# Kernel optimization log

Hardware: AMD Instinct MI355X
Metric: run time of the kernel (lower is better)

## Reference

```python
import math
import jax, jax.numpy as jnp
import numpy as np

D_MODEL = 1024
N_HEADS = 16
D_HEAD = D_MODEL // N_HEADS
ROPE_BASE = 10000.0
MAX_SEQ_LEN = 2048


def build_cos_sin_cache(d_head, max_seq_len, base=ROPE_BASE):
    half = d_head // 2
    i = jnp.arange(half, dtype=jnp.float32)
    theta = 1.0 / (base ** (2.0 * i / d_head))  # (half,)
    t = jnp.arange(max_seq_len, dtype=jnp.float32)
    angles = jnp.outer(t, theta)  # (T, half)
    return jnp.cos(angles), jnp.sin(angles)


def rotate_half(x):
    d = x.shape[-1]
    x1, x2 = x[..., : d // 2], x[..., d // 2 :]
    return jnp.concatenate([-x2, x1], axis=-1)


def apply_rope(x, cos_t, sin_t):
    # x: (..., T, d_head); cos_t/sin_t: (T, d_head//2)
    cos_full = jnp.concatenate([cos_t, cos_t], axis=-1)
    sin_full = jnp.concatenate([sin_t, sin_t], axis=-1)
    return x * cos_full + rotate_half(x) * sin_full


def setup_inputs() -> dict:
    key = jax.random.key(0)
    ks = jax.random.split(key, 5)
    B, T = 2, 2048
    s = 1.0 / math.sqrt(D_MODEL)
    return {
        "x": jax.random.normal(ks[0], (B, T, D_MODEL), dtype=jnp.float32),
        "Wq": jax.random.normal(ks[1], (D_MODEL, D_MODEL), dtype=jnp.float32) * s,
        "Wk": jax.random.normal(ks[2], (D_MODEL, D_MODEL), dtype=jnp.float32) * s,
        "Wv": jax.random.normal(ks[3], (D_MODEL, D_MODEL), dtype=jnp.float32) * s,
        "Wo": jax.random.normal(ks[4], (D_MODEL, D_MODEL), dtype=jnp.float32) * s,
    }


def reference(x, Wq, Wk, Wv, Wo):
    B, T, _ = x.shape
    # Linear with torch weight convention: y = x @ W.T
    q = jnp.einsum("btd,ed->bte", x, Wq)
    k = jnp.einsum("btd,ed->bte", x, Wk)
    v = jnp.einsum("btd,ed->bte", x, Wv)
    # (B, H, T, d_head)
    q = q.reshape(B, T, N_HEADS, D_HEAD).transpose(0, 2, 1, 3)
    k = k.reshape(B, T, N_HEADS, D_HEAD).transpose(0, 2, 1, 3)
    v = v.reshape(B, T, N_HEADS, D_HEAD).transpose(0, 2, 1, 3)
    cos_c, sin_c = build_cos_sin_cache(D_HEAD, MAX_SEQ_LEN)
    cos_t, sin_t = cos_c[:T], sin_c[:T]
    q = apply_rope(q, cos_t, sin_t)
    k = apply_rope(k, cos_t, sin_t)
    scale = math.sqrt(D_HEAD)
    scores = jnp.einsum("bhqd,bhkd->bhqk", q, k) / scale
    causal = jnp.triu(jnp.full((T, T), -jnp.inf, dtype=x.dtype), k=1)
    scores = scores + causal
    weights = jax.nn.softmax(scores, axis=-1)
    out = jnp.einsum("bhqk,bhkd->bhqd", weights, v)
    out = out.transpose(0, 2, 1, 3).reshape(B, T, D_MODEL)
    return jnp.einsum("btd,ed->bte", out, Wo)
```

## Files before the change

kernel.cpp:

```cpp
#include <hip/hip_runtime.h>
#include <stdint.h>
#include <math.h>

typedef __attribute__((ext_vector_type(8))) short short8;
typedef __attribute__((ext_vector_type(4))) float f32x4;
typedef __attribute__((ext_vector_type(16))) float f32x16;

#define T_SEQ 2048
#define MROWS 4096
#define LOG2E 1.44269504088896f

#define OFF_XBF   ((size_t)0)
#define OFF_WQ    ((size_t)8388608)
#define OFF_WK    ((size_t)10485760)
#define OFF_WV    ((size_t)12582912)
#define OFF_WO    ((size_t)14680064)
#define OFF_Q     ((size_t)16777216)
#define OFF_K     ((size_t)25165824)
#define OFF_VT    ((size_t)33554432)
#define OFF_ATT   ((size_t)41943040)
#define OFF_COS   ((size_t)50331648)
#define OFF_SIN   ((size_t)50593792)
#define OFF_OPART ((size_t)0)
#define OFF_ML    ((size_t)12582912)

__device__ __forceinline__ unsigned short f2bf(float f) {
  unsigned u = __float_as_uint(f);
  u += 0x7fffu + ((u >> 16) & 1u);
  return (unsigned short)(u >> 16);
}

__device__ __forceinline__ float bf2f(unsigned short u) {
  return __uint_as_float((unsigned)u << 16);
}

__device__ __forceinline__ void gld_lds16(const void* g, void* l) {
  __builtin_amdgcn_global_load_lds(
      (__attribute__((address_space(1))) void*)(g),
      (__attribute__((address_space(3))) void*)(l), 16, 0, 0);
}

__device__ __forceinline__ unsigned cvt_pk_bf16(float lo, float hi) {
  unsigned r;
  asm("v_cvt_pk_bf16_f32 %0, %1, %2" : "=v"(r) : "v"(lo), "v"(hi));
  return r;
}

__global__ void prep_kernel(const float* x, const float* wq, const float* wk,
                            const float* wv, const float* wo, char* ws) {
  const size_t NX4 = (size_t)MROWS * 1024 / 4;
  const size_t NW4 = (size_t)1024 * 1024 / 4;
  const size_t NT = (size_t)T_SEQ * 32;
  unsigned short* xb = (unsigned short*)(ws + OFF_XBF);
  unsigned short* wqb = (unsigned short*)(ws + OFF_WQ);
  unsigned short* wkb = (unsigned short*)(ws + OFF_WK);
  unsigned short* wvb = (unsigned short*)(ws + OFF_WV);
  unsigned short* wob = (unsigned short*)(ws + OFF_WO);
  float* cosb = (float*)(ws + OFF_COS);
  float* sinb = (float*)(ws + OFF_SIN);
  size_t nvec = NX4 + 4 * NW4;
  size_t total = nvec + NT;
  for (size_t i = (size_t)blockIdx.x * blockDim.x + threadIdx.x; i < total;
       i += (size_t)gridDim.x * blockDim.x) {
    if (i < nvec) {
      const float* src;
      unsigned short* dst;
      size_t e;
      if (i < NX4) {
        src = x; dst = xb; e = i * 4;
      } else {
        size_t j = i - NX4;
        int wsel = (int)(j / NW4);
        e = (j - (size_t)wsel * NW4) * 4;
        src = wsel == 0 ? wq : wsel == 1 ? wk : wsel == 2 ? wv : wo;
        dst = wsel == 0 ? wqb : wsel == 1 ? wkb : wsel == 2 ? wvb : wob;
      }
      float4 v = *(const float4*)(src + e);
      unsigned long long p =
          (unsigned long long)f2bf(v.x) |
          ((unsigned long long)f2bf(v.y) << 16) |
          ((unsigned long long)f2bf(v.z) << 32) |
          ((unsigned long long)f2bf(v.w) << 48);
      *(unsigned long long*)(dst + e) = p;
    } else {
      size_t j = i - nvec;
      int t = (int)(j >> 5), ii = (int)(j & 31);
      double th = exp(-(double)ii * (9.210340371976184 / 32.0));
      float ang = (float)t * (float)th;
      cosb[j] = cosf(ang);
      sinb[j] = sinf(ang);
    }
  }
}

__global__ __launch_bounds__(256, 3) void gemm_qkv(
    const unsigned short* Abf, const unsigned short* Wall, unsigned short* qkout,
    unsigned short* vtout, const float* cosT, const float* sinT) {
  const int K = 1024;
  int bid0 = blockIdx.x;
  int bid = (bid0 & 7) * 96 + (bid0 >> 3);
  int bm = bid / 24, bn = bid % 24;
  int sel = bn >> 3, bnc = bn & 7;
  int tid = threadIdx.x;
  int l = tid & 63, w = tid >> 6;
  int wm = w >> 1, wn = w & 1;
  int g = l >> 4;

  __shared__ __align__(16) char ldsbuf[32768];

  auto stage = [&](int kt, int buf) {
    int base = buf * 16384;
#pragma unroll
    for (int i = 0; i < 2; ++i) {
      int p = (w * 2 + i) * 1024;
      int row = (p >> 6) + (l >> 2);
      int u = l & 3;
      const char* ga = (const char*)Abf +
          ((size_t)(bm * 128 + row) * K + (size_t)kt * 32) * 2 + u * 16;
      gld_lds16(ga, ldsbuf + base + p);
      const char* gb = (const char*)Wall +
          ((size_t)(bn * 128 + row) * K + (size_t)kt * 32) * 2 + u * 16;
      gld_lds16(gb, ldsbuf + base + 8192 + p);
    }
  };

  f32x4 acc[4][4] = {};
  stage(0, 0);
  const int nk = K / 32;
  for (int kt = 0; kt < nk; ++kt) {
    int buf = kt & 1;
    if (kt + 1 < nk) {
      stage(kt + 1, buf ^ 1);
      asm volatile("s_waitcnt vmcnt(4)" ::: "memory");
    } else {
      asm volatile("s_waitcnt vmcnt(0)" ::: "memory");
    }
    __builtin_amdgcn_s_barrier();
    __builtin_amdgcn_sched_barrier(0);
    const char* Ab = ldsbuf + buf * 16384;
    const char* Bb = Ab + 8192;
    short8 af[4], bfr[4];
#pragma unroll
    for (int m = 0; m < 4; ++m)
      af[m] = *(const short8*)(Ab + (wm * 64 + m * 16 + (l & 15)) * 64 + g * 16);
#pragma unroll
    for (int n = 0; n < 4; ++n)
      bfr[n] = *(const short8*)(Bb + (wn * 64 + n * 16 + (l & 15)) * 64 + g * 16);
#pragma unroll
    for (int m = 0; m < 4; ++m)
#pragma unroll
      for (int n = 0; n < 4; ++n)
        acc[m][n] = __builtin_amdgcn_mfma_f32_16x16x32_bf16(af[m], bfr[n],
                                                            acc[m][n], 0, 0, 0);
    __builtin_amdgcn_s_barrier();
  }

  int row0 = bm * 128 + wm * 64;
  int col0 = bnc * 128 + wn * 64;
  if (sel < 2) {
    float qscale = sel == 0 ? 0.125f * LOG2E : 1.0f;
    unsigned short* C = qkout + (size_t)sel * MROWS * 1024;
#pragma unroll
    for (int m = 0; m < 4; ++m)
#pragma unroll
      for (int n = 0; n < 2; ++n)
#pragma unroll
        for (int r = 0; r < 4; ++r) {
          int row = row0 + m * 16 + g * 4 + r;
          int t = row & (T_SEQ - 1);
          int d = n * 16 + (l & 15);
          float c = cosT[t * 32 + d], s = sinT[t * 32 + d];
          float v0 = acc[m][n][r], v1 = acc[m][n + 2][r];
          C[(size_t)row * 1024 + col0 + d] = f2bf((v0 * c - v1 * s) * qscale);
          C[(size_t)row * 1024 + col0 + d + 32] = f2bf((v1 * c + v0 * s) * qscale);
        }
  } else {
    unsigned short* C = vtout;
#pragma unroll
    for (int m = 0; m < 4; ++m) {
      int rowb = row0 + m * 16 + g * 4;
      int bb = rowb >> 11, t0 = rowb & (T_SEQ - 1);
#pragma unroll
      for (int n = 0; n < 4; ++n) {
        int e = col0 + n * 16 + (l & 15);
        unsigned long long pv =
            (unsigned long long)f2bf(acc[m][n][0]) |
            ((unsigned long long)f2bf(acc[m][n][1]) << 16) |
            ((unsigned long long)f2bf(acc[m][n][2]) << 32) |
            ((unsigned long long)f2bf(acc[m][n][3]) << 48);
        *(unsigned long long*)(C + ((size_t)bb * 1024 + e) * T_SEQ + t0) = pv;
      }
    }
  }
}

__global__ __launch_bounds__(256, 3) void gemm_wo(const unsigned short* Abf,
                                                  const unsigned short* Wbf,
                                                  float* out) {
  const int K = 1024, N = 1024;
  int bid0 = blockIdx.x;
  int bid = (bid0 & 7) * 64 + (bid0 >> 3);
  int bm = bid >> 4, bn = bid & 15;
  int tid = threadIdx.x;
  int l = tid & 63, w = tid >> 6;
  int wm = w >> 1, wn = w & 1;
  int g = l >> 4;

  __shared__ __align__(16) char ldsbuf[24576];

  auto stage = [&](int kt, int buf) {
    char* base = ldsbuf + buf * 12288;
#pragma unroll
    for (int i = 0; i < 2; ++i) {
      int pos = tid + i * 256;
      int row = pos >> 2, u = pos & 3;
      const char* ga = (const char*)Abf +
          ((size_t)(bm * 128 + row) * K + (size_t)kt * 32) * 2 + u * 16;
      gld_lds16(ga, base + row * 64 + u * 16);
    }
    {
      int row = tid >> 2, u = tid & 3;
      const char* gb = (const char*)Wbf +
          ((size_t)(bn * 64 + row) * K + (size_t)kt * 32) * 2 + u * 16;
      gld_lds16(gb, base + 8192 + row * 64 + u * 16);
    }
  };

  f32x4 acc[4][2] = {};
  stage(0, 0);
  const int nk = K / 32;
  for (int kt = 0; kt < nk; ++kt) {
    int buf = kt & 1;
    if (kt + 1 < nk) {
      stage(kt + 1, buf ^ 1);
      asm volatile("s_waitcnt vmcnt(3)" ::: "memory");
    } else {
      asm volatile("s_waitcnt vmcnt(0)" ::: "memory");
    }
    __builtin_amdgcn_s_barrier();
    __builtin_amdgcn_sched_barrier(0);
    const char* Ab = ldsbuf + buf * 12288;
    const char* Bb = Ab + 8192;
    short8 af[4], bfr[2];
#pragma unroll
    for (int m = 0; m < 4; ++m)
      af[m] = *(const short8*)(Ab + (wm * 64 + m * 16 + (l & 15)) * 64 + g * 16);
#pragma unroll
    for (int n = 0; n < 2; ++n)
      bfr[n] = *(const short8*)(Bb + (wn * 32 + n * 16 + (l & 15)) * 64 + g * 16);
#pragma unroll
    for (int m = 0; m < 4; ++m)
#pragma unroll
      for (int n = 0; n < 2; ++n)
        acc[m][n] = __builtin_amdgcn_mfma_f32_16x16x32_bf16(af[m], bfr[n],
                                                            acc[m][n], 0, 0, 0);
    __builtin_amdgcn_s_barrier();
  }

  int row0 = bm * 128 + wm * 64;
  int col0 = bn * 64 + wn * 32;
#pragma unroll
  for (int m = 0; m < 4; ++m)
#pragma unroll
    for (int n = 0; n < 2; ++n)
#pragma unroll
      for (int r = 0; r < 4; ++r)
        out[(size_t)(row0 + m * 16 + g * 4 + r) * N + col0 + n * 16 + (l & 15)] =
            acc[m][n][r];
}

__global__ __launch_bounds__(256, 2) void attn_kernel(
    const unsigned short* Qbf, const unsigned short* Kbf,
    const unsigned short* VT, unsigned short* att,
    unsigned short* Opart, float* lpart) {
  static const unsigned char qtab[24] = {15, 15, 14, 14, 7,  13, 13, 12,
                                         12, 6,  11, 11, 10, 10, 5,  9,
                                         9,  8,  8,  4,  3,  2,  1,  0};
  static const unsigned char stab[24] = {0,   1,   0,   1,   255, 0,   1,   0,
                                         1,   255, 0,   1,   0,   1,   255, 0,
                                         1,   0,   1,   255, 255, 255, 255, 255};
  int bid = blockIdx.x;
  int bh = bid & 31;
  int cid = bid >> 5;
  int qt = qtab[cid];
  int sv = stab[cid];
  int ns = (sv == 255) ? 1 : 2;
  int s = (sv == 255) ? 0 : sv;
  int b = bh >> 4, h = bh & 15;
  int ntt = 2 * qt + 2;
  int ntb = (ns == 2) ? (ntt >> 1) : ntt;
  int kt0 = s * ntb;
  int hp = (ntb + 1) >> 1;

  int tid = threadIdx.x;
  int pr = tid >> 7;
  int t127 = tid & 127;
  int l = tid & 63, wv = (tid >> 6) & 1;
  int q32 = l & 31, hi = l >> 5;
  int q0 = qt * 128;
  int q0w = q0 + wv * 64;
  int myCnt = pr ? (ntb - hp) : hp;
  int myKt0 = kt0 + (pr ? hp : 0);
  int ntw = ((q0w + 63) >> 6) + 1 - myKt0;
  if (ntw > myCnt) ntw = myCnt;
  if (ntw < 0) ntw = 0;
  int pbi = (ns == 2) ? (bh * 16 + (qt - 8) * 2 + s) : 0;

  __shared__ __align__(16) char lds[2][2][16384];

  short8 qfA[4], qfB[4];
  {
    const char* qb = (const char*)Qbf +
        ((size_t)(b * T_SEQ + q0w + q32)) * 2048 + h * 128 + hi * 16;
#pragma unroll
    for (int ks = 0; ks < 4; ++ks) {
      qfA[ks] = *(const short8*)(qb + ks * 32);
      qfB[ks] = *(const short8*)(qb + 32 * 2048 + ks * 32);
    }
  }
  asm volatile("s_waitcnt vmcnt(0)" ::: "memory");

  auto stage = [&](int gt, int buf) {
    char* Kd = &lds[pr][buf][0];
    char* Vd = &lds[pr][buf][8192];
    int colb = (t127 & 7) * 16;
#pragma unroll
    for (int r = 0; r < 4; ++r) {
      int d = (t127 >> 3) + r * 16;
      int sc = colb ^ ((d & 7) << 4);
      const char* gk = (const char*)Kbf +
          ((size_t)(b * T_SEQ + gt * 64 + d)) * 2048 + h * 128 + sc;
      gld_lds16(gk, Kd + d * 128 + colb);
      const char* gv = (const char*)VT +
          ((size_t)(b * 1024 + h * 64 + d)) * 4096 + gt * 128 + sc;
      gld_lds16(gv, Vd + d * 128 + colb);
    }
  };

  f32x16 oA0 = {}, oA1 = {}, oB0 = {}, oB1 = {};
  float lA = 0.f, lB = 0.f;
  stage(myKt0, 0);
  for (int it = 0; it < hp; ++it) {
    int buf = it & 1;
    if (it + 1 < myCnt) {
      stage(myKt0 + it + 1, buf ^ 1);
      asm volatile("s_waitcnt vmcnt(8)" ::: "memory");
    } else {
      asm volatile("s_waitcnt vmcnt(0)" ::: "memory");
    }
    __builtin_amdgcn_s_barrier();
    __builtin_amdgcn_sched_barrier(0);
    if (it < ntw) {
      int gt = myKt0 + it;
      const char* Kl = &lds[pr][buf][0];
      const char* Vl = &lds[pr][buf][8192];

      f32x16 sA0 = {}, sA1 = {}, sB0 = {}, sB1 = {};
      __builtin_amdgcn_s_setprio(1);
#pragma unroll
      for (int ks = 0; ks < 4; ++ks) {
        int sc = (ks * 32 + hi * 16) ^ ((q32 & 7) << 4);
        short8 k0 = *(const short8*)(Kl + q32 * 128 + sc);
        short8 k1 = *(const short8*)(Kl + (q32 + 32) * 128 + sc);
        sA0 = __builtin_amdgcn_mfma_f32_32x32x16_bf16(k0, qfA[ks], sA0, 0, 0, 0);
        sA1 = __builtin_amdgcn_mfma_f32_32x32x16_bf16(k1, qfA[ks], sA1, 0, 0, 0);
        sB0 = __builtin_amdgcn_mfma_f32_32x32x16_bf16(k0, qfB[ks], sB0, 0, 0, 0);
        sB1 = __builtin_amdgcn_mfma_f32_32x32x16_bf16(k1, qfB[ks], sB1, 0, 0, 0);
      }
      __builtin_amdgcn_s_setprio(0);

      if (gt * 64 + 63 > q0w) {
        int qA = q0w + q32, qB = qA + 32;
#pragma unroll
        for (int r = 0; r < 16; ++r) {
          int kkb = gt * 64 + (r & 3) + 8 * (r >> 2) + 4 * hi;
          if (kkb > qA) sA0[r] = -1e30f;
          if (kkb + 32 > qA) sA1[r] = -1e30f;
          if (kkb > qB) sB0[r] = -1e30f;
          if (kkb + 32 > qB) sB1[r] = -1e30f;
        }
      }

      float lsA = 0.f, lsB = 0.f;
#pragma unroll
      for (int r = 0; r < 16; ++r) {
        sA0[r] = __builtin_amdgcn_exp2f(sA0[r]);
        sA1[r] = __builtin_amdgcn_exp2f(sA1[r]);
        sB0[r] = __builtin_amdgcn_exp2f(sB0[r]);
        sB1[r] = __builtin_amdgcn_exp2f(sB1[r]);
        lsA += sA0[r] + sA1[r];
        lsB += sB0[r] + sB1[r];
      }
      lA += lsA;
      lB += lsB;

      short8 pbA[4], pbB[4];
#pragma unroll
      for (int ks = 0; ks < 4; ++ks) {
        union { unsigned u[4]; short8 s8; } ua, ub;
#pragma unroll
        for (int j = 0; j < 4; ++j) {
          int bse = (ks & 1) * 8 + 2 * j;
          float a0 = (ks & 2) ? sA1[bse] : sA0[bse];
          float a1 = (ks & 2) ? sA1[bse + 1] : sA0[bse + 1];
          ua.u[j] = cvt_pk_bf16(a0, a1);
          float b0 = (ks & 2) ? sB1[bse] : sB0[bse];
          float b1 = (ks & 2) ? sB1[bse + 1] : sB0[bse + 1];
          ub.u[j] = cvt_pk_bf16(b0, b1);
        }
        pbA[ks] = ua.s8;
        pbB[ks] = ub.s8;
      }

      __builtin_amdgcn_s_setprio(1);
#pragma unroll
      for (int ks = 0; ks < 4; ++ks) {
        int sp = (q32 & 7) << 4;
        int cA = (ks * 32 + 8 * hi) ^ sp;
        int cB = (ks * 32 + 16 + 8 * hi) ^ sp;
#pragma unroll
        for (int cc = 0; cc < 2; ++cc) {
          int dv = cc * 32 + q32;
          union { unsigned long long u[2]; short8 s8; } vv;
          vv.u[0] = *(const unsigned long long*)(Vl + dv * 128 + cA);
          vv.u[1] = *(const unsigned long long*)(Vl + dv * 128 + cB);
          if (cc == 0) {
            oA0 = __builtin_amdgcn_mfma_f32_32x32x16_bf16(vv.s8, pbA[ks], oA0, 0, 0, 0);
            oB0 = __builtin_amdgcn_mfma_f32_32x32x16_bf16(vv.s8, pbB[ks], oB0, 0, 0, 0);
          } else {
            oA1 = __builtin_amdgcn_mfma_f32_32x32x16_bf16(vv.s8, pbA[ks], oA1, 0, 0, 0);
            oB1 = __builtin_amdgcn_mfma_f32_32x32x16_bf16(vv.s8, pbB[ks], oB1, 0, 0, 0);
          }
        }
      }
      __builtin_amdgcn_s_setprio(0);
    }
    __builtin_amdgcn_s_barrier();
  }

  lA += __shfl_xor(lA, 32);
  lB += __shfl_xor(lB, 32);

  float* M = (float*)(&lds[1][0][0]);
  float* Ll = (float*)(&lds[0][0][0]);
  __syncthreads();
  if (pr == 1) {
#pragma unroll
    for (int grp = 0; grp < 2; ++grp)
#pragma unroll
      for (int cc = 0; cc < 2; ++cc)
#pragma unroll
        for (int r = 0; r < 16; ++r) {
          int d = cc * 32 + (r & 3) + 8 * (r >> 2) + 4 * hi;
          float v = grp == 0 ? (cc ? oA1[r] : oA0[r]) : (cc ? oB1[r] : oB0[r]);
          M[(wv * 2 + grp) * 2048 + q32 * 64 + (d ^ (q32 & 31))] = v;
        }
    if (hi == 0) {
      Ll[wv * 128 + q32] = lA;
      Ll[wv * 128 + 64 + q32] = lB;
    }
  }
  __syncthreads();
  if (pr == 0) {
#pragma unroll
    for (int grp = 0; grp < 2; ++grp)
#pragma unroll
      for (int cc = 0; cc < 2; ++cc)
#pragma unroll
        for (int r = 0; r < 16; ++r) {
          int d = cc * 32 + (r & 3) + 8 * (r >> 2) + 4 * hi;
          float v = M[(wv * 2 + grp) * 2048 + q32 * 64 + (d ^ (q32 & 31))];
          if (grp == 0) { if (cc) oA1[r] += v; else oA0[r] += v; }
          else          { if (cc) oB1[r] += v; else oB0[r] += v; }
        }
    lA += Ll[wv * 128 + q32];
    lB += Ll[wv * 128 + 64 + q32];
  }
  __syncthreads();

  float* Ol = (float*)(&lds[0][0][0]);
  if (pr == 0) {
    float scA = (ns == 1) ? (1.0f / lA) : 1.0f;
    float scB = (ns == 1) ? (1.0f / lB) : 1.0f;
    if (ns > 1 && hi == 0) {
      lpart[(size_t)pbi * 128 + wv * 64 + q32] = lA;
      lpart[(size_t)pbi * 128 + wv * 64 + 32 + q32] = lB;
    }
#pragma unroll
    for (int grp = 0; grp < 2; ++grp)
#pragma unroll
      for (int cc = 0; cc < 2; ++cc)
#pragma unroll
        for (int r = 0; r < 16; ++r) {
          int d = cc * 32 + (r & 3) + 8 * (r >> 2) + 4 * hi;
          float v;
          if (grp == 0) v = (cc ? oA1[r] : oA0[r]) * scA;
          else          v = (cc ? oB1[r] : oB0[r]) * scB;
          Ol[(wv * 2 + grp) * 2048 + q32 * 64 + (d ^ (q32 & 31))] = v;
        }
  }
  __syncthreads();

#pragma unroll
  for (int i = 0; i < 4; ++i) {
    int idx2 = tid + i * 256;
    int row = idx2 >> 3;
    int seg = idx2 & 7;
    int q = row & 31, rg = row >> 5;
    unsigned short tmp[8];
#pragma unroll
    for (int j = 0; j < 8; ++j) {
      int d = seg * 8 + j;
      tmp[j] = f2bf(Ol[rg * 2048 + q * 64 + (d ^ (q & 31))]);
    }
    if (ns == 1) {
      *(unsigned long long*)(att + ((size_t)(b * T_SEQ + q0 + row)) * 1024 +
                             h * 64 + seg * 8) = *(unsigned long long*)&tmp[0];
      *(unsigned long long*)(att + ((size_t)(b * T_SEQ + q0 + row)) * 1024 +
                             h * 64 + seg * 8 + 4) = *(unsigned long long*)&tmp[4];
    } else {
      *(unsigned long long*)(Opart + ((size_t)pbi * 128 + row) * 64 + seg * 8) =
          *(unsigned long long*)&tmp[0];
      *(unsigned long long*)(Opart + ((size_t)pbi * 128 + row) * 64 + seg * 8 + 4) =
          *(unsigned long long*)&tmp[4];
    }
  }
}

__global__ __launch_bounds__(256) void combine_kernel(
    const unsigned short* Opart, const float* lpart, unsigned short* att) {
  int blk = blockIdx.x;
  int bh = blk & 31, j = blk >> 5;
  int qt = 8 + j;
  int b = bh >> 4, h = bh & 15;
  int q0 = qt * 128;
  int pbi0 = bh * 16 + j * 2;
#pragma unroll
  for (int i = 0; i < 4; ++i) {
    int u = threadIdx.x + i * 256;
    int q = u >> 3, seg = u & 7;
    float lsum = lpart[(size_t)pbi0 * 128 + q] +
                 lpart[(size_t)(pbi0 + 1) * 128 + q];
    float inv = 1.0f / lsum;
    short8 o0 = *(const short8*)(Opart + ((size_t)pbi0 * 128 + q) * 64 + seg * 8);
    short8 o1 =
        *(const short8*)(Opart + ((size_t)(pbi0 + 1) * 128 + q) * 64 + seg * 8);
    union { unsigned short us[8]; short8 s8; } r;
#pragma unroll
    for (int k = 0; k < 8; ++k)
      r.us[k] = f2bf((bf2f((unsigned short)o0[k]) +
                      bf2f((unsigned short)o1[k])) * inv);
    *(short8*)(att + ((size_t)(b * T_SEQ + q0 + q)) * 1024 + h * 64 + seg * 8) =
        r.s8;
  }
}

extern "C" void kernel_launch(void* const* d_in, const int* in_sizes, int n_in,
                              void* d_out, int out_size, void* d_ws,
                              size_t ws_size, hipStream_t stream) {
  const float* x = (const float*)d_in[0];
  const float* Wq = (const float*)d_in[1];
  const float* Wk = (const float*)d_in[2];
  const float* Wv = (const float*)d_in[3];
  const float* Wo = (const float*)d_in[4];
  char* ws = (char*)d_ws;

  unsigned short* xb = (unsigned short*)(ws + OFF_XBF);
  unsigned short* wall = (unsigned short*)(ws + OFF_WQ);
  unsigned short* wob = (unsigned short*)(ws + OFF_WO);
  unsigned short* qbf = (unsigned short*)(ws + OFF_Q);
  unsigned short* vtb = (unsigned short*)(ws + OFF_VT);
  unsigned short* att = (unsigned short*)(ws + OFF_ATT);
  unsigned short* kbf = (unsigned short*)(ws + OFF_K);
  unsigned short* opart = (unsigned short*)(ws + OFF_OPART);
  float* lp = (float*)(ws + OFF_ML);
  const float* cosT = (const float*)(ws + OFF_COS);
  const float* sinT = (const float*)(ws + OFF_SIN);

  prep_kernel<<<2048, 256, 0, stream>>>(x, Wq, Wk, Wv, Wo, ws);
  gemm_qkv<<<768, 256, 0, stream>>>(xb, wall, qbf, vtb, cosT, sinT);
  attn_kernel<<<768, 256, 0, stream>>>(qbf, kbf, vtb, att, opart, lp);
  combine_kernel<<<256, 256, 0, stream>>>(opart, lp, att);
  gemm_wo<<<512, 256, 0, stream>>>(att, wob, (float*)d_out);
}
```

Baseline: 104.9 us.

## Drop split-KV attention and combine kernel, use one block per query tile

Replaces the split-KV work decomposition for long query tiles, where two blocks each handled half the keys and a separate combine kernel merged the partials, with a single block per (batch, head, query tile). Blocks are ordered longest-first so heavy tiles start early. This removes one kernel launch, the partial-output and l-sum traffic, and the extra bf16 rounding of partials. The cost is less parallelism: 512 blocks instead of 768, so the longest tiles set a longer critical path and load balance across CUs may be worse.

```diff
diff --git a/kernel.cpp b/kernel.cpp
--- a/kernel.cpp
+++ b/kernel.cpp
@@ -21,17 +21,11 @@
 #define OFF_ATT   ((size_t)41943040)
 #define OFF_COS   ((size_t)50331648)
 #define OFF_SIN   ((size_t)50593792)
-#define OFF_OPART ((size_t)0)
-#define OFF_ML    ((size_t)12582912)
 
 __device__ __forceinline__ unsigned short f2bf(float f) {
   unsigned u = __float_as_uint(f);
   u += 0x7fffu + ((u >> 16) & 1u);
   return (unsigned short)(u >> 16);
-}
-
-__device__ __forceinline__ float bf2f(unsigned short u) {
-  return __uint_as_float((unsigned)u << 16);
 }
 
 __device__ __forceinline__ void gld_lds16(const void* g, void* l) {
@@ -271,26 +265,14 @@
 
 __global__ __launch_bounds__(256, 2) void attn_kernel(
     const unsigned short* Qbf, const unsigned short* Kbf,
-    const unsigned short* VT, unsigned short* att,
-    unsigned short* Opart, float* lpart) {
-  static const unsigned char qtab[24] = {15, 15, 14, 14, 7,  13, 13, 12,
-                                         12, 6,  11, 11, 10, 10, 5,  9,
-                                         9,  8,  8,  4,  3,  2,  1,  0};
-  static const unsigned char stab[24] = {0,   1,   0,   1,   255, 0,   1,   0,
-                                         1,   255, 0,   1,   0,   1,   255, 0,
-                                         1,   0,   1,   255, 255, 255, 255, 255};
+    const unsigned short* VT, unsigned short* att) {
   int bid = blockIdx.x;
   int bh = bid & 31;
-  int cid = bid >> 5;
-  int qt = qtab[cid];
-  int sv = stab[cid];
-  int ns = (sv == 255) ? 1 : 2;
-  int s = (sv == 255) ? 0 : sv;
+  int idx = bid >> 5;
+  int qt = idx < 8 ? (15 - idx) : (idx - 8);
   int b = bh >> 4, h = bh & 15;
   int ntt = 2 * qt + 2;
-  int ntb = (ns == 2) ? (ntt >> 1) : ntt;
-  int kt0 = s * ntb;
-  int hp = (ntb + 1) >> 1;
+  int hp = ntt >> 1;
 
   int tid = threadIdx.x;
   int pr = tid >> 7;
@@ -299,12 +281,10 @@
   int q32 = l & 31, hi = l >> 5;
   int q0 = qt * 128;
   int q0w = q0 + wv * 64;
-  int myCnt = pr ? (ntb - hp) : hp;
-  int myKt0 = kt0 + (pr ? hp : 0);
+  int myKt0 = pr ? hp : 0;
   int ntw = ((q0w + 63) >> 6) + 1 - myKt0;
-  if (ntw > myCnt) ntw = myCnt;
+  if (ntw > hp) ntw = hp;
   if (ntw < 0) ntw = 0;
-  int pbi = (ns == 2) ? (bh * 16 + (qt - 8) * 2 + s) : 0;
 
   __shared__ __align__(16) char lds[2][2][16384];
 
@@ -342,7 +322,7 @@
   stage(myKt0, 0);
   for (int it = 0; it < hp; ++it) {
     int buf = it & 1;
-    if (it + 1 < myCnt) {
+    if (it + 1 < hp) {
       stage(myKt0 + it + 1, buf ^ 1);
       asm volatile("s_waitcnt vmcnt(8)" ::: "memory");
     } else {
@@ -480,12 +460,8 @@
 
   float* Ol = (float*)(&lds[0][0][0]);
   if (pr == 0) {
-    float scA = (ns == 1) ? (1.0f / lA) : 1.0f;
-    float scB = (ns == 1) ? (1.0f / lB) : 1.0f;
-    if (ns > 1 && hi == 0) {
-      lpart[(size_t)pbi * 128 + wv * 64 + q32] = lA;
-      lpart[(size_t)pbi * 128 + wv * 64 + 32 + q32] = lB;
-    }
+    float scA = 1.0f / lA;
+    float scB = 1.0f / lB;
 #pragma unroll
     for (int grp = 0; grp < 2; ++grp)
 #pragma unroll
@@ -513,45 +489,10 @@
       int d = seg * 8 + j;
       tmp[j] = f2bf(Ol[rg * 2048 + q * 64 + (d ^ (q & 31))]);
     }
-    if (ns == 1) {
-      *(unsigned long long*)(att + ((size_t)(b * T_SEQ + q0 + row)) * 1024 +
-                             h * 64 + seg * 8) = *(unsigned long long*)&tmp[0];
-      *(unsigned long long*)(att + ((size_t)(b * T_SEQ + q0 + row)) * 1024 +
-                             h * 64 + seg * 8 + 4) = *(unsigned long long*)&tmp[4];
-    } else {
-      *(unsigned long long*)(Opart + ((size_t)pbi * 128 + row) * 64 + seg * 8) =
-          *(unsigned long long*)&tmp[0];
-      *(unsigned long long*)(Opart + ((size_t)pbi * 128 + row) * 64 + seg * 8 + 4) =
-          *(unsigned long long*)&tmp[4];
-    }
-  }
-}
-
-__global__ __launch_bounds__(256) void combine_kernel(
-    const unsigned short* Opart, const float* lpart, unsigned short* att) {
-  int blk = blockIdx.x;
-  int bh = blk & 31, j = blk >> 5;
-  int qt = 8 + j;
-  int b = bh >> 4, h = bh & 15;
-  int q0 = qt * 128;
-  int pbi0 = bh * 16 + j * 2;
-#pragma unroll
-  for (int i = 0; i < 4; ++i) {
-    int u = threadIdx.x + i * 256;
-    int q = u >> 3, seg = u & 7;
-    float lsum = lpart[(size_t)pbi0 * 128 + q] +
-                 lpart[(size_t)(pbi0 + 1) * 128 + q];
-    float inv = 1.0f / lsum;
-    short8 o0 = *(const short8*)(Opart + ((size_t)pbi0 * 128 + q) * 64 + seg * 8);
-    short8 o1 =
-        *(const short8*)(Opart + ((size_t)(pbi0 + 1) * 128 + q) * 64 + seg * 8);
-    union { unsigned short us[8]; short8 s8; } r;
-#pragma unroll
-    for (int k = 0; k < 8; ++k)
-      r.us[k] = f2bf((bf2f((unsigned short)o0[k]) +
-                      bf2f((unsigned short)o1[k])) * inv);
-    *(short8*)(att + ((size_t)(b * T_SEQ + q0 + q)) * 1024 + h * 64 + seg * 8) =
-        r.s8;
+    *(unsigned long long*)(att + ((size_t)(b * T_SEQ + q0 + row)) * 1024 +
+                           h * 64 + seg * 8) = *(unsigned long long*)&tmp[0];
+    *(unsigned long long*)(att + ((size_t)(b * T_SEQ + q0 + row)) * 1024 +
+                           h * 64 + seg * 8 + 4) = *(unsigned long long*)&tmp[4];
   }
 }
 
@@ -572,14 +513,11 @@
   unsigned short* vtb = (unsigned short*)(ws + OFF_VT);
   unsigned short* att = (unsigned short*)(ws + OFF_ATT);
   unsigned short* kbf = (unsigned short*)(ws + OFF_K);
-  unsigned short* opart = (unsigned short*)(ws + OFF_OPART);
-  float* lp = (float*)(ws + OFF_ML);
   const float* cosT = (const float*)(ws + OFF_COS);
   const float* sinT = (const float*)(ws + OFF_SIN);
 
   prep_kernel<<<2048, 256, 0, stream>>>(x, Wq, Wk, Wv, Wo, ws);
   gemm_qkv<<<768, 256, 0, stream>>>(xb, wall, qbf, vtb, cosT, sinT);
-  attn_kernel<<<768, 256, 0, stream>>>(qbf, kbf, vtb, att, opart, lp);
-  combine_kernel<<<256, 256, 0, stream>>>(opart, lp, att);
+  attn_kernel<<<512, 256, 0, stream>>>(qbf, kbf, vtb, att);
   gemm_wo<<<512, 256, 0, stream>>>(att, wob, (float*)d_out);
 }
```

Result: faster. 99.42 us (-5.2%).
